# Performance work log

Measured on AMD Instinct MI355X. Metric: run time of the kernel, lower is better.

The kernel has to match this reference:

```python
import jax, jax.numpy as jnp
import numpy as np

EPS = 1e-6  # SublayerConnection LayerNorm eps (annotated-transformer style)
NEG = -1e9
NUM_USED = 3  # used_domain_list = ['news','book','iwslt'] -> mask indices 0,1,2


def _layer_norm(x, scale, bias):
    m = jnp.mean(x, axis=-1, keepdims=True)
    v = jnp.mean(jnp.square(x - m), axis=-1, keepdims=True)
    return (x - m) * jax.lax.rsqrt(v + EPS) * scale + bias


def setup_inputs() -> dict:
    key = jax.random.key(0)
    ks = jax.random.split(key, 8)
    B, L, H, F, D = 8, 1024, 1024, 2048, 4
    s = 0.02
    return {
        "x": jax.random.normal(ks[0], (B, L, H), jnp.float32),
        "domain_mask": jnp.array([1, 1, 1, 0], jnp.int32),
        "gate_w1": jax.random.normal(ks[1], (H, D), jnp.float32) * s,
        "gate_b1": jnp.zeros((D,), jnp.float32),
        "gate_w2": jax.random.normal(ks[2], (D, D), jnp.float32) * s,
        "gate_b2": jnp.zeros((D,), jnp.float32),
        "ln_s_book": jnp.ones((H,), jnp.float32),
        "ln_b_book": jnp.zeros((H,), jnp.float32),
        "ln_s_iwslt": jnp.ones((H,), jnp.float32),
        "ln_b_iwslt": jnp.zeros((H,), jnp.float32),
        "ad_w1": jax.random.normal(ks[3], (H, F), jnp.float32) * s,
        "ad_b1": jnp.zeros((F,), jnp.float32),
        "ad_w2": jax.random.normal(ks[4], (F, H), jnp.float32) * s,
        "ad_b2": jnp.zeros((H,), jnp.float32),
    }


def reference(x, domain_mask, gate_w1, gate_b1, gate_w2, gate_b2,
              ln_s_book, ln_b_book, ln_s_iwslt, ln_b_iwslt,
              ad_w1, ad_b1, ad_w2, ad_b2):
    # inner gate for target_domain='book': Linear -> ReLU -> Linear, masked softmax
    h = jnp.maximum(jnp.einsum('blh,hd->bld', x, gate_w1) + gate_b1, 0.0)
    logits = jnp.einsum('bld,de->ble', h, gate_w2) + gate_b2          # [B,L,Dmax]
    logits = jnp.where(domain_mask == 0, NEG, logits)
    prob = jax.nn.softmax(logits, axis=-1)
    weights = prob[..., :NUM_USED]                                     # [B,L,3]

    # per-domain wo_residual adapter (dropout identity at eval).
    # Faithful quirk: both domains use target_domain ('book') adapter weights,
    # but each domain's own SublayerConnection LayerNorm params.
    def adapt(ln_s, ln_b):
        z = _layer_norm(x, ln_s, ln_b)
        z = jnp.maximum(jnp.einsum('blh,hf->blf', z, ad_w1) + ad_b1, 0.0)
        return jnp.einsum('blf,fh->blh', z, ad_w2) + ad_b2

    outs = jnp.stack([x, adapt(ln_s_book, ln_b_book),
                      adapt(ln_s_iwslt, ln_b_iwslt)], axis=-1)         # [B,L,H,3]
    mix = jnp.einsum('blhd,bld->blh', outs, weights)
    return x + mix
```

## Files before the change

### kernel.cpp

```cpp
#include <hip/hip_runtime.h>
#include <stdint.h>

typedef __attribute__((ext_vector_type(8))) short bf16x8;
typedef __attribute__((ext_vector_type(4))) float f32x4;

__device__ __forceinline__ unsigned short f2bf(float f) {
  union { float f; unsigned u; } v; v.f = f;
  unsigned r = v.u + 0x7fffu + ((v.u >> 16) & 1u);
  return (unsigned short)(r >> 16);
}
__device__ __forceinline__ float bf2f(unsigned short u) {
  union { unsigned u; float f; } v; v.u = ((unsigned)u) << 16; return v.f;
}
__device__ __forceinline__ void gload16(const void* g, void* l) {
  __builtin_amdgcn_global_load_lds(
      (const __attribute__((address_space(1))) unsigned int*)(uintptr_t)g,
      (__attribute__((address_space(3))) unsigned int*)(uintptr_t)l,
      16, 0, 0);
}

__global__ __launch_bounds__(256)
void k_gate_ln(const float* __restrict__ x, const int* __restrict__ dmask,
               const float* __restrict__ gw1, const float* __restrict__ gb1,
               const float* __restrict__ gw2, const float* __restrict__ gb2,
               const float* __restrict__ sb, const float* __restrict__ bb,
               const float* __restrict__ si, const float* __restrict__ bi,
               float* __restrict__ wout,
               unsigned short* __restrict__ z)
{
  const int row = blockIdx.x;
  const int t = threadIdx.x;
  const int wave = t >> 6, lane = t & 63;
  const float4 xv = *(const float4*)(x + (size_t)row * 1024 + t * 4);
  const float xs[4] = {xv.x, xv.y, xv.z, xv.w};

  float v[6];
  v[0] = v[1] = v[2] = v[3] = 0.f;
#pragma unroll
  for (int j = 0; j < 4; ++j) {
    const float4 w = *(const float4*)(gw1 + (size_t)(t * 4 + j) * 4);
    v[0] += xs[j] * w.x; v[1] += xs[j] * w.y; v[2] += xs[j] * w.z; v[3] += xs[j] * w.w;
  }
  v[4] = xs[0] + xs[1] + xs[2] + xs[3];
  v[5] = xs[0]*xs[0] + xs[1]*xs[1] + xs[2]*xs[2] + xs[3]*xs[3];

#pragma unroll
  for (int off = 32; off > 0; off >>= 1)
#pragma unroll
    for (int c = 0; c < 6; ++c) v[c] += __shfl_down(v[c], off, 64);

  __shared__ float wsum[4][6];
  __shared__ float bc[2];
  if (lane == 0)
#pragma unroll
    for (int c = 0; c < 6; ++c) wsum[wave][c] = v[c];
  __syncthreads();
  if (t == 0) {
    float r[6];
#pragma unroll
    for (int c = 0; c < 6; ++c) r[c] = wsum[0][c] + wsum[1][c] + wsum[2][c] + wsum[3][c];
    float h0 = fmaxf(r[0] + gb1[0], 0.f);
    float h1 = fmaxf(r[1] + gb1[1], 0.f);
    float h2 = fmaxf(r[2] + gb1[2], 0.f);
    float h3 = fmaxf(r[3] + gb1[3], 0.f);
    float lg[4];
#pragma unroll
    for (int e = 0; e < 4; ++e) {
      float val = h0*gw2[0*4+e] + h1*gw2[1*4+e] + h2*gw2[2*4+e] + h3*gw2[3*4+e] + gb2[e];
      lg[e] = (dmask[e] == 0) ? -1.0e9f : val;
    }
    float m = fmaxf(fmaxf(lg[0], lg[1]), fmaxf(lg[2], lg[3]));
    float e0 = expf(lg[0]-m), e1 = expf(lg[1]-m), e2 = expf(lg[2]-m), e3 = expf(lg[3]-m);
    float inv = 1.f / (e0 + e1 + e2 + e3);
    float4 wv; wv.x = e0*inv; wv.y = e1*inv; wv.z = e2*inv; wv.w = 0.f;
    *(float4*)(wout + (size_t)row * 4) = wv;
    float mean = r[4] * (1.f/1024.f);
    float var  = r[5] * (1.f/1024.f) - mean * mean;
    bc[0] = mean; bc[1] = rsqrtf(var + 1e-6f);
  }
  __syncthreads();
  const float mean = bc[0], rstd = bc[1];

  const float4 sbv = *(const float4*)(sb + t*4);
  const float4 bbv = *(const float4*)(bb + t*4);
  const float4 siv = *(const float4*)(si + t*4);
  const float4 biv = *(const float4*)(bi + t*4);
  const float sbs[4] = {sbv.x, sbv.y, sbv.z, sbv.w};
  const float bbs[4] = {bbv.x, bbv.y, bbv.z, bbv.w};
  const float sis[4] = {siv.x, siv.y, siv.z, siv.w};
  const float bis[4] = {biv.x, biv.y, biv.z, biv.w};
  ushort4 zb, zi;
  unsigned short zbv[4], ziv[4];
#pragma unroll
  for (int j = 0; j < 4; ++j) {
    float xn = (xs[j] - mean) * rstd;
    zbv[j] = f2bf(xn * sbs[j] + bbs[j]);
    ziv[j] = f2bf(xn * sis[j] + bis[j]);
  }
  zb.x = zbv[0]; zb.y = zbv[1]; zb.z = zbv[2]; zb.w = zbv[3];
  zi.x = ziv[0]; zi.y = ziv[1]; zi.z = ziv[2]; zi.w = ziv[3];
  *(ushort4*)(z + (size_t)(2 * row) * 1024 + t * 4) = zb;
  *(ushort4*)(z + (size_t)(2 * row + 1) * 1024 + t * 4) = zi;
}

__global__ __launch_bounds__(256)
void k_transpose_bf16(const float* __restrict__ src, unsigned short* __restrict__ dst,
                      int R, int C)
{
  __shared__ float tile[32][33];
  const int tx = threadIdx.x & 31, ty = threadIdx.x >> 5;
  const int c0 = blockIdx.x * 32, r0 = blockIdx.y * 32;
#pragma unroll
  for (int j = 0; j < 32; j += 8)
    tile[ty + j][tx] = src[(size_t)(r0 + ty + j) * C + c0 + tx];
  __syncthreads();
#pragma unroll
  for (int j = 0; j < 32; j += 8)
    dst[(size_t)(c0 + ty + j) * R + r0 + tx] = f2bf(tile[tx][ty + j]);
}

template <int MODE, int K, int NBX>
__global__ __launch_bounds__(512, 2)
void gemm256(const unsigned short* __restrict__ A,
             const unsigned short* __restrict__ Bt,
             const float* __restrict__ bias,
             unsigned short* __restrict__ Cb,
             const float* __restrict__ x,
             const float* __restrict__ wgt,
             float* __restrict__ outp)
{
  constexpr int NKT = K / 64;
  constexpr int N = NBX * 256;
  __shared__ __align__(16) char lds[131072];

  const int tid = threadIdx.x;
  const int wave = tid >> 6, lane = tid & 63;
  const int lr = lane & 15, lk = lane >> 4;
  const int wm = wave >> 2, wn = wave & 3;

  const int cpx = (int)gridDim.x >> 3;
  const int flat = (int)blockIdx.x;
  const int swz = (flat & 7) * cpx + (flat >> 3);
  const int bm0 = (swz / NBX) * 256;
  const int bn0 = (swz % NBX) * 256;

  const int srow = tid >> 3;
  const int schunk = ((tid & 7) ^ (srow & 7)) * 8;
  const unsigned short* aSrc = A + (size_t)(bm0 + srow) * K + schunk;
  const unsigned short* bSrc = Bt + (size_t)(bn0 + srow) * K + schunk;
  const int ldsWaveOff = wave * 1024;

  const int xorv = (lr & 7) << 4;
  const int koff0 = (lk * 16) ^ xorv;
  const int koff1 = (64 + lk * 16) ^ xorv;
  const int arowB = wm * 128 + lr;
  const int browB = wn * 64 + lr;

  f32x4 acc[8][4] = {};

  auto stage = [&](int j) {
    if (j >= 4 * NKT) return;
    const int tile = j >> 2, h = j & 3;
    const unsigned short* s = (h < 2 ? bSrc : aSrc) + (size_t)((h & 1) * 128) * K + tile * 64;
    char* d = lds + ((tile & 1) << 16) + ((h < 2) ? 32768 : 0) + ((h & 1) << 14) + ldsWaveOff;
    gload16(s, d);
    gload16(s + (size_t)64 * K, d + 8192);
  };

  stage(0); stage(1); stage(2); stage(3); stage(4); stage(5);
  asm volatile("s_waitcnt vmcnt(4)" ::: "memory");
  __builtin_amdgcn_s_barrier();

#pragma unroll 2
  for (int t = 0; t < NKT; ++t) {
    const char* curA = lds + ((t & 1) << 16);
    const char* curB = curA + 32768;
    const int jb = 6 + 4 * t;
    bf16x8 bf[4][2];
    bf16x8 af[2][2];

#pragma unroll
    for (int q = 0; q < 4; ++q) {
      if (q == 0) {
#pragma unroll
        for (int ni = 0; ni < 4; ++ni) {
          bf[ni][0] = *(const bf16x8*)(curB + (browB + ni * 16) * 128 + koff0);
          bf[ni][1] = *(const bf16x8*)(curB + (browB + ni * 16) * 128 + koff1);
        }
      }
#pragma unroll
      for (int i = 0; i < 2; ++i) {
        af[i][0] = *(const bf16x8*)(curA + (arowB + (2 * q + i) * 16) * 128 + koff0);
        af[i][1] = *(const bf16x8*)(curA + (arowB + (2 * q + i) * 16) * 128 + koff1);
      }
      stage(jb + q);
      if (q == 3) {
        if (t < NKT - 2)       asm volatile("s_waitcnt vmcnt(4)" ::: "memory");
        else if (t == NKT - 2) asm volatile("s_waitcnt vmcnt(0)" ::: "memory");
      }
      __builtin_amdgcn_s_barrier();
      asm volatile("s_waitcnt lgkmcnt(0)" ::: "memory");
      __builtin_amdgcn_s_setprio(1);
#pragma unroll
      for (int i = 0; i < 2; ++i)
#pragma unroll
        for (int ni = 0; ni < 4; ++ni) {
          acc[2 * q + i][ni] = __builtin_amdgcn_mfma_f32_16x16x32_bf16(af[i][0], bf[ni][0], acc[2 * q + i][ni], 0, 0, 0);
          acc[2 * q + i][ni] = __builtin_amdgcn_mfma_f32_16x16x32_bf16(af[i][1], bf[ni][1], acc[2 * q + i][ni], 0, 0, 0);
        }
      __builtin_amdgcn_s_setprio(0);
    }
  }

  __syncthreads();

  if (MODE == 0) {
#pragma unroll
    for (int ni = 0; ni < 4; ++ni) {
      const int colb = (wn * 64 + ni * 16 + lr) * 2;
      const float bv = bias[bn0 + wn * 64 + ni * 16 + lr];
#pragma unroll
      for (int mi = 0; mi < 8; ++mi) {
#pragma unroll
        for (int j = 0; j < 4; ++j) {
          const int row = wm * 128 + mi * 16 + lk * 4 + j;
          float v = fmaxf(acc[mi][ni][j] + bv, 0.f);
          *(unsigned short*)(lds + row * 512 + (colb ^ ((row & 7) << 4))) = f2bf(v);
        }
      }
    }
    __syncthreads();
#pragma unroll
    for (int s = 0; s < 16; ++s) {
      const int row = wave * 32 + s * 2 + (lane >> 5);
      const int c = lane & 31;
      bf16x8 vv = *(const bf16x8*)(lds + row * 512 + ((c * 16) ^ ((row & 7) << 4)));
      *(bf16x8*)(Cb + (size_t)(bm0 + row) * N + bn0 + c * 8) = vv;
    }
  } else {
    const int orbase = bm0 >> 1;
#pragma unroll
    for (int mi = 0; mi < 8; ++mi) {
      const int lr0 = wm * 64 + mi * 8 + lk * 2;
      const float4 wa = *(const float4*)(wgt + (size_t)(orbase + lr0) * 4);
      const float4 wb = *(const float4*)(wgt + (size_t)(orbase + lr0 + 1) * 4);
#pragma unroll
      for (int ni = 0; ni < 4; ++ni) {
        const int colb = (wn * 64 + ni * 16 + lr) * 4;
        const float bv = bias[bn0 + wn * 64 + ni * 16 + lr];
        float m0 = wa.y * (acc[mi][ni][0] + bv) + wa.z * (acc[mi][ni][1] + bv);
        float m1 = wb.y * (acc[mi][ni][2] + bv) + wb.z * (acc[mi][ni][3] + bv);
        *(float*)(lds + (size_t)lr0 * 1024 + (colb ^ ((lr0 & 6) << 5))) = m0;
        *(float*)(lds + (size_t)(lr0 + 1) * 1024 + (colb ^ (((lr0 + 1) & 6) << 5))) = m1;
      }
    }
    __syncthreads();
#pragma unroll
    for (int s = 0; s < 16; ++s) {
      const int lrow = wave * 16 + s;
      const int gor = orbase + lrow;
      f32x4 m = *(const f32x4*)(lds + (size_t)lrow * 1024 + ((lane * 16) ^ ((lrow & 6) << 5)));
      const float4 xv = *(const float4*)(x + (size_t)gor * 1024 + bn0 + lane * 4);
      const float w0 = wgt[(size_t)gor * 4];
      f32x4 o;
      o[0] = xv.x * (1.f + w0) + m[0];
      o[1] = xv.y * (1.f + w0) + m[1];
      o[2] = xv.z * (1.f + w0) + m[2];
      o[3] = xv.w * (1.f + w0) + m[3];
      *(f32x4*)(outp + (size_t)gor * 1024 + bn0 + lane * 4) = o;
    }
  }
}

extern "C" void kernel_launch(void* const* d_in, const int* in_sizes, int n_in,
                              void* d_out, int out_size, void* d_ws, size_t ws_size,
                              hipStream_t stream) {
  const float* x    = (const float*)d_in[0];
  const int*   dm   = (const int*)  d_in[1];
  const float* gw1  = (const float*)d_in[2];
  const float* gb1  = (const float*)d_in[3];
  const float* gw2  = (const float*)d_in[4];
  const float* gb2  = (const float*)d_in[5];
  const float* lsb  = (const float*)d_in[6];
  const float* lbb  = (const float*)d_in[7];
  const float* lsi  = (const float*)d_in[8];
  const float* lbi  = (const float*)d_in[9];
  const float* aw1  = (const float*)d_in[10];
  const float* ab1  = (const float*)d_in[11];
  const float* aw2  = (const float*)d_in[12];
  const float* ab2  = (const float*)d_in[13];
  float* out = (float*)d_out;

  char* ws = (char*)d_ws;
  float*          wgt  = (float*)(ws + 0);
  unsigned short* z    = (unsigned short*)(ws + 131072);
  unsigned short* w1t  = (unsigned short*)(ws + 131072 + 33554432);
  unsigned short* w2t  = (unsigned short*)(ws + 131072 + 33554432 + 4194304);
  unsigned short* hbuf = (unsigned short*)(ws + 131072 + 33554432 + 8388608);

  k_gate_ln<<<8192, 256, 0, stream>>>(x, dm, gw1, gb1, gw2, gb2,
                                      lsb, lbb, lsi, lbi, wgt, z);
  k_transpose_bf16<<<dim3(2048/32, 1024/32), 256, 0, stream>>>(aw1, w1t, 1024, 2048);
  k_transpose_bf16<<<dim3(1024/32, 2048/32), 256, 0, stream>>>(aw2, w2t, 2048, 1024);
  gemm256<0, 1024, 8><<<512, 512, 0, stream>>>(z, w1t, ab1, hbuf, nullptr, nullptr, nullptr);
  gemm256<1, 2048, 4><<<256, 512, 0, stream>>>(hbuf, w2t, ab2, nullptr, x, wgt, out);
}
```

Before: 261.3 us.

## Use one wave per row in gate/LN kernel and restructure GEMM K-loop pipeline

The gate+LayerNorm kernel now gives each 64-lane wave a whole row, so reductions are done with xor shuffles and the block-level shared memory and barriers go away. The GEMM main loop drops the staggered per-quarter staging with a barrier every quarter. It now prefetches the whole next K tile at the start of each iteration and double-buffers A fragments in registers around MFMA groups, with one wait and barrier per tile. This cuts barrier count but the prefetch lead is shorter, which may expose more global load latency.

```diff
diff --git a/kernel.cpp b/kernel.cpp
--- a/kernel.cpp
+++ b/kernel.cpp
@@ -28,79 +28,74 @@
                float* __restrict__ wout,
                unsigned short* __restrict__ z)
 {
-  const int row = blockIdx.x;
-  const int t = threadIdx.x;
-  const int wave = t >> 6, lane = t & 63;
-  const float4 xv = *(const float4*)(x + (size_t)row * 1024 + t * 4);
-  const float xs[4] = {xv.x, xv.y, xv.z, xv.w};
-
-  float v[6];
-  v[0] = v[1] = v[2] = v[3] = 0.f;
+  const int lane = threadIdx.x & 63;
+  const int row = blockIdx.x * 4 + (threadIdx.x >> 6);
+  const float* xr = x + (size_t)row * 1024;
+
+  float4 xv[4];
+  float p0 = 0.f, p1 = 0.f, p2 = 0.f, p3 = 0.f, s = 0.f, ss = 0.f;
 #pragma unroll
   for (int j = 0; j < 4; ++j) {
-    const float4 w = *(const float4*)(gw1 + (size_t)(t * 4 + j) * 4);
-    v[0] += xs[j] * w.x; v[1] += xs[j] * w.y; v[2] += xs[j] * w.z; v[3] += xs[j] * w.w;
-  }
-  v[4] = xs[0] + xs[1] + xs[2] + xs[3];
-  v[5] = xs[0]*xs[0] + xs[1]*xs[1] + xs[2]*xs[2] + xs[3]*xs[3];
-
-#pragma unroll
-  for (int off = 32; off > 0; off >>= 1)
-#pragma unroll
-    for (int c = 0; c < 6; ++c) v[c] += __shfl_down(v[c], off, 64);
-
-  __shared__ float wsum[4][6];
-  __shared__ float bc[2];
-  if (lane == 0)
-#pragma unroll
-    for (int c = 0; c < 6; ++c) wsum[wave][c] = v[c];
-  __syncthreads();
-  if (t == 0) {
-    float r[6];
-#pragma unroll
-    for (int c = 0; c < 6; ++c) r[c] = wsum[0][c] + wsum[1][c] + wsum[2][c] + wsum[3][c];
-    float h0 = fmaxf(r[0] + gb1[0], 0.f);
-    float h1 = fmaxf(r[1] + gb1[1], 0.f);
-    float h2 = fmaxf(r[2] + gb1[2], 0.f);
-    float h3 = fmaxf(r[3] + gb1[3], 0.f);
-    float lg[4];
-#pragma unroll
-    for (int e = 0; e < 4; ++e) {
-      float val = h0*gw2[0*4+e] + h1*gw2[1*4+e] + h2*gw2[2*4+e] + h3*gw2[3*4+e] + gb2[e];
-      lg[e] = (dmask[e] == 0) ? -1.0e9f : val;
-    }
-    float m = fmaxf(fmaxf(lg[0], lg[1]), fmaxf(lg[2], lg[3]));
-    float e0 = expf(lg[0]-m), e1 = expf(lg[1]-m), e2 = expf(lg[2]-m), e3 = expf(lg[3]-m);
-    float inv = 1.f / (e0 + e1 + e2 + e3);
-    float4 wv; wv.x = e0*inv; wv.y = e1*inv; wv.z = e2*inv; wv.w = 0.f;
+    const int i0 = lane * 4 + j * 256;
+    xv[j] = *(const float4*)(xr + i0);
+    const float xc[4] = {xv[j].x, xv[j].y, xv[j].z, xv[j].w};
+#pragma unroll
+    for (int c = 0; c < 4; ++c) {
+      const float4 w = *(const float4*)(gw1 + (size_t)(i0 + c) * 4);
+      p0 += xc[c] * w.x; p1 += xc[c] * w.y; p2 += xc[c] * w.z; p3 += xc[c] * w.w;
+      s += xc[c]; ss += xc[c] * xc[c];
+    }
+  }
+#pragma unroll
+  for (int m = 32; m >= 1; m >>= 1) {
+    p0 += __shfl_xor(p0, m, 64); p1 += __shfl_xor(p1, m, 64);
+    p2 += __shfl_xor(p2, m, 64); p3 += __shfl_xor(p3, m, 64);
+    s  += __shfl_xor(s,  m, 64); ss += __shfl_xor(ss, m, 64);
+  }
+  const float h0 = fmaxf(p0 + gb1[0], 0.f), h1 = fmaxf(p1 + gb1[1], 0.f);
+  const float h2 = fmaxf(p2 + gb1[2], 0.f), h3 = fmaxf(p3 + gb1[3], 0.f);
+  float lg[4];
+#pragma unroll
+  for (int e = 0; e < 4; ++e) {
+    float val = h0 * gw2[e] + h1 * gw2[4 + e] + h2 * gw2[8 + e] + h3 * gw2[12 + e] + gb2[e];
+    lg[e] = (dmask[e] == 0) ? -1.0e9f : val;
+  }
+  const float mx = fmaxf(fmaxf(lg[0], lg[1]), fmaxf(lg[2], lg[3]));
+  const float e0 = expf(lg[0] - mx), e1 = expf(lg[1] - mx);
+  const float e2 = expf(lg[2] - mx), e3 = expf(lg[3] - mx);
+  const float inv = 1.f / (e0 + e1 + e2 + e3);
+  if (lane == 0) {
+    float4 wv; wv.x = e0 * inv; wv.y = e1 * inv; wv.z = e2 * inv; wv.w = 0.f;
     *(float4*)(wout + (size_t)row * 4) = wv;
-    float mean = r[4] * (1.f/1024.f);
-    float var  = r[5] * (1.f/1024.f) - mean * mean;
-    bc[0] = mean; bc[1] = rsqrtf(var + 1e-6f);
-  }
-  __syncthreads();
-  const float mean = bc[0], rstd = bc[1];
-
-  const float4 sbv = *(const float4*)(sb + t*4);
-  const float4 bbv = *(const float4*)(bb + t*4);
-  const float4 siv = *(const float4*)(si + t*4);
-  const float4 biv = *(const float4*)(bi + t*4);
-  const float sbs[4] = {sbv.x, sbv.y, sbv.z, sbv.w};
-  const float bbs[4] = {bbv.x, bbv.y, bbv.z, bbv.w};
-  const float sis[4] = {siv.x, siv.y, siv.z, siv.w};
-  const float bis[4] = {biv.x, biv.y, biv.z, biv.w};
-  ushort4 zb, zi;
-  unsigned short zbv[4], ziv[4];
+  }
+  const float mean = s * (1.f / 1024.f);
+  const float rstd = rsqrtf(ss * (1.f / 1024.f) - mean * mean + 1e-6f);
+
 #pragma unroll
   for (int j = 0; j < 4; ++j) {
-    float xn = (xs[j] - mean) * rstd;
-    zbv[j] = f2bf(xn * sbs[j] + bbs[j]);
-    ziv[j] = f2bf(xn * sis[j] + bis[j]);
-  }
-  zb.x = zbv[0]; zb.y = zbv[1]; zb.z = zbv[2]; zb.w = zbv[3];
-  zi.x = ziv[0]; zi.y = ziv[1]; zi.z = ziv[2]; zi.w = ziv[3];
-  *(ushort4*)(z + (size_t)(2 * row) * 1024 + t * 4) = zb;
-  *(ushort4*)(z + (size_t)(2 * row + 1) * 1024 + t * 4) = zi;
+    const int i0 = lane * 4 + j * 256;
+    const float4 sbv = *(const float4*)(sb + i0);
+    const float4 bbv = *(const float4*)(bb + i0);
+    const float4 siv = *(const float4*)(si + i0);
+    const float4 biv = *(const float4*)(bi + i0);
+    const float xc[4] = {xv[j].x, xv[j].y, xv[j].z, xv[j].w};
+    const float sbs[4] = {sbv.x, sbv.y, sbv.z, sbv.w};
+    const float bbs[4] = {bbv.x, bbv.y, bbv.z, bbv.w};
+    const float sis[4] = {siv.x, siv.y, siv.z, siv.w};
+    const float bis[4] = {biv.x, biv.y, biv.z, biv.w};
+    ushort4 zb, zi;
+    unsigned short zbv[4], ziv[4];
+#pragma unroll
+    for (int c = 0; c < 4; ++c) {
+      const float xn = (xc[c] - mean) * rstd;
+      zbv[c] = f2bf(xn * sbs[c] + bbs[c]);
+      ziv[c] = f2bf(xn * sis[c] + bis[c]);
+    }
+    zb.x = zbv[0]; zb.y = zbv[1]; zb.z = zbv[2]; zb.w = zbv[3];
+    zi.x = ziv[0]; zi.y = ziv[1]; zi.z = ziv[2]; zi.w = ziv[3];
+    *(ushort4*)(z + (size_t)(2 * row) * 1024 + i0) = zb;
+    *(ushort4*)(z + (size_t)(2 * row + 1) * 1024 + i0) = zi;
+  }
 }
 
 __global__ __launch_bounds__(256)
@@ -118,6 +113,25 @@
   for (int j = 0; j < 32; j += 8)
     dst[(size_t)(c0 + ty + j) * R + r0 + tx] = f2bf(tile[tx][ty + j]);
 }
+
+#define LOADA(dst, q) do {                                                            \
+  dst[0][0] = *(const bf16x8*)(curA + (arowB + (2*(q)+0)*16) * 128 + koff0);          \
+  dst[0][1] = *(const bf16x8*)(curA + (arowB + (2*(q)+0)*16) * 128 + koff1);          \
+  dst[1][0] = *(const bf16x8*)(curA + (arowB + (2*(q)+1)*16) * 128 + koff0);          \
+  dst[1][1] = *(const bf16x8*)(curA + (arowB + (2*(q)+1)*16) * 128 + koff1);          \
+} while (0)
+
+#define MFMAQ(src, q) do {                                                            \
+  __builtin_amdgcn_s_setprio(1);                                                      \
+  _Pragma("unroll")                                                                   \
+  for (int i = 0; i < 2; ++i) {                                                       \
+    _Pragma("unroll")                                                                 \
+    for (int ni = 0; ni < 4; ++ni) {                                                  \
+      acc[2*(q)+i][ni] = __builtin_amdgcn_mfma_f32_16x16x32_bf16(src[i][0], bf[ni][0], acc[2*(q)+i][ni], 0, 0, 0); \
+      acc[2*(q)+i][ni] = __builtin_amdgcn_mfma_f32_16x16x32_bf16(src[i][1], bf[ni][1], acc[2*(q)+i][ni], 0, 0, 0); \
+    } }                                                                               \
+  __builtin_amdgcn_s_setprio(0);                                                      \
+} while (0)
 
 template <int MODE, int K, int NBX>
 __global__ __launch_bounds__(512, 2)
@@ -158,58 +172,42 @@
 
   f32x4 acc[8][4] = {};
 
-  auto stage = [&](int j) {
-    if (j >= 4 * NKT) return;
-    const int tile = j >> 2, h = j & 3;
-    const unsigned short* s = (h < 2 ? bSrc : aSrc) + (size_t)((h & 1) * 128) * K + tile * 64;
-    char* d = lds + ((tile & 1) << 16) + ((h < 2) ? 32768 : 0) + ((h & 1) << 14) + ldsWaveOff;
-    gload16(s, d);
-    gload16(s + (size_t)64 * K, d + 8192);
+  auto stage_tile = [&](int tt) {
+#pragma unroll
+    for (int h = 0; h < 4; ++h) {
+      const unsigned short* sp = (h < 2 ? bSrc : aSrc) + (size_t)((h & 1) * 128) * K + tt * 64;
+      char* d = lds + ((tt & 1) << 16) + ((h < 2) ? 32768 : 0) + ((h & 1) << 14) + ldsWaveOff;
+      gload16(sp, d);
+      gload16(sp + (size_t)64 * K, d + 8192);
+    }
   };
 
-  stage(0); stage(1); stage(2); stage(3); stage(4); stage(5);
-  asm volatile("s_waitcnt vmcnt(4)" ::: "memory");
+  stage_tile(0);
+  asm volatile("s_waitcnt vmcnt(0)" ::: "memory");
   __builtin_amdgcn_s_barrier();
 
 #pragma unroll 2
   for (int t = 0; t < NKT; ++t) {
     const char* curA = lds + ((t & 1) << 16);
     const char* curB = curA + 32768;
-    const int jb = 6 + 4 * t;
+    if (t + 1 < NKT) stage_tile(t + 1);
+
     bf16x8 bf[4][2];
-    bf16x8 af[2][2];
-
-#pragma unroll
-    for (int q = 0; q < 4; ++q) {
-      if (q == 0) {
-#pragma unroll
-        for (int ni = 0; ni < 4; ++ni) {
-          bf[ni][0] = *(const bf16x8*)(curB + (browB + ni * 16) * 128 + koff0);
-          bf[ni][1] = *(const bf16x8*)(curB + (browB + ni * 16) * 128 + koff1);
-        }
-      }
-#pragma unroll
-      for (int i = 0; i < 2; ++i) {
-        af[i][0] = *(const bf16x8*)(curA + (arowB + (2 * q + i) * 16) * 128 + koff0);
-        af[i][1] = *(const bf16x8*)(curA + (arowB + (2 * q + i) * 16) * 128 + koff1);
-      }
-      stage(jb + q);
-      if (q == 3) {
-        if (t < NKT - 2)       asm volatile("s_waitcnt vmcnt(4)" ::: "memory");
-        else if (t == NKT - 2) asm volatile("s_waitcnt vmcnt(0)" ::: "memory");
-      }
-      __builtin_amdgcn_s_barrier();
-      asm volatile("s_waitcnt lgkmcnt(0)" ::: "memory");
-      __builtin_amdgcn_s_setprio(1);
-#pragma unroll
-      for (int i = 0; i < 2; ++i)
-#pragma unroll
-        for (int ni = 0; ni < 4; ++ni) {
-          acc[2 * q + i][ni] = __builtin_amdgcn_mfma_f32_16x16x32_bf16(af[i][0], bf[ni][0], acc[2 * q + i][ni], 0, 0, 0);
-          acc[2 * q + i][ni] = __builtin_amdgcn_mfma_f32_16x16x32_bf16(af[i][1], bf[ni][1], acc[2 * q + i][ni], 0, 0, 0);
-        }
-      __builtin_amdgcn_s_setprio(0);
-    }
+#pragma unroll
+    for (int ni = 0; ni < 4; ++ni) {
+      bf[ni][0] = *(const bf16x8*)(curB + (browB + ni * 16) * 128 + koff0);
+      bf[ni][1] = *(const bf16x8*)(curB + (browB + ni * 16) * 128 + koff1);
+    }
+    bf16x8 a0[2][2], a1[2][2];
+    LOADA(a0, 0);
+    LOADA(a1, 1);
+    MFMAQ(a0, 0);  LOADA(a0, 2);
+    MFMAQ(a1, 1);  LOADA(a1, 3);
+    MFMAQ(a0, 2);
+    MFMAQ(a1, 3);
+
+    asm volatile("s_waitcnt vmcnt(0)" ::: "memory");
+    __builtin_amdgcn_s_barrier();
   }
 
   __syncthreads();
@@ -231,8 +229,8 @@
     }
     __syncthreads();
 #pragma unroll
-    for (int s = 0; s < 16; ++s) {
-      const int row = wave * 32 + s * 2 + (lane >> 5);
+    for (int sx = 0; sx < 16; ++sx) {
+      const int row = wave * 32 + sx * 2 + (lane >> 5);
       const int c = lane & 31;
       bf16x8 vv = *(const bf16x8*)(lds + row * 512 + ((c * 16) ^ ((row & 7) << 4)));
       *(bf16x8*)(Cb + (size_t)(bm0 + row) * N + bn0 + c * 8) = vv;
@@ -256,8 +254,8 @@
     }
     __syncthreads();
 #pragma unroll
-    for (int s = 0; s < 16; ++s) {
-      const int lrow = wave * 16 + s;
+    for (int sx = 0; sx < 16; ++sx) {
+      const int lrow = wave * 16 + sx;
       const int gor = orbase + lrow;
       f32x4 m = *(const f32x4*)(lds + (size_t)lrow * 1024 + ((lane * 16) ^ ((lrow & 6) << 5)));
       const float4 xv = *(const float4*)(x + (size_t)gor * 1024 + bn0 + lane * 4);
@@ -298,7 +296,7 @@
   unsigned short* w2t  = (unsigned short*)(ws + 131072 + 33554432 + 4194304);
   unsigned short* hbuf = (unsigned short*)(ws + 131072 + 33554432 + 8388608);
 
-  k_gate_ln<<<8192, 256, 0, stream>>>(x, dm, gw1, gb1, gw2, gb2,
+  k_gate_ln<<<2048, 256, 0, stream>>>(x, dm, gw1, gb1, gw2, gb2,
                                       lsb, lbb, lsi, lbi, wgt, z);
   k_transpose_bf16<<<dim3(2048/32, 1024/32), 256, 0, stream>>>(aw1, w1t, 1024, 2048);
   k_transpose_bf16<<<dim3(1024/32, 2048/32), 256, 0, stream>>>(aw2, w2t, 2048, 1024);
```

After: 258.8 us. Within noise of the previous version (-1.0%).
